# Optimization experiments

Measured on AMD Instinct MI355X. Metric: run time of the kernel, lower is better.

## Reference

```python
import jax, jax.numpy as jnp
import numpy as np

EMD_DIM = 64
NB_EMD = 512


def setup_inputs() -> dict:
    key = jax.random.key(0)
    k_x, k_e = jax.random.split(key)
    x = jax.random.normal(k_x, (32, 64, 64, EMD_DIM), dtype=jnp.float32)
    # codebook buffer, shape [emd_dim, nb_emd] as in the torch module
    embed = jax.random.normal(k_e, (EMD_DIM, NB_EMD), dtype=jnp.float32)
    return {"x": x, "embed": embed}


def reference(x, embed):
    # Eval-mode forward (the EMA buffer update only runs under self.training
    # and does not affect this forward's outputs).
    flatten = x.reshape(-1, EMD_DIM)                      # [N, d]
    dist = (jnp.sum(flatten * flatten, axis=1, keepdims=True)
            - 2.0 * flatten @ embed
            + jnp.sum(embed * embed, axis=0, keepdims=True))  # [N, K]
    emd_id_flat = jnp.argmax(-dist, axis=1)               # nearest code index [N]
    emd_id = emd_id_flat.reshape(x.shape[:-1])            # [B, H, W]
    q = jnp.take(embed.T, emd_id, axis=0)                 # gather codes -> [B,H,W,d]
    diff = jnp.mean((jax.lax.stop_gradient(q) - x) ** 2)  # commitment loss
    q_st = x + jax.lax.stop_gradient(q - x)               # straight-through
    return (q_st, diff, emd_id)
```

## Files before the change

### kernel.cpp

```cpp
#include <hip/hip_runtime.h>

#define N_VEC 131072
#define K 512
#define D 64
#define GUARD 0.05f
#define NB_GATHER 2048
#define FB_Q 16

typedef __attribute__((ext_vector_type(8))) short bf16x8;
typedef __attribute__((ext_vector_type(4))) float f32x4;

#define PIN(v) asm("" : "+v"(v))

static __device__ __forceinline__ short f2bf(float f) {
  unsigned u = __builtin_bit_cast(unsigned, f);
  u += 0x7fffu + ((u >> 16) & 1u);
  return (short)(u >> 16);
}
static __device__ __forceinline__ float bf2f(short h) {
  unsigned u = ((unsigned)(unsigned short)h) << 16;
  return __builtin_bit_cast(float, u);
}
static __device__ __forceinline__ void split8(const float4 f0, const float4 f1,
                                              bf16x8& h, bf16x8& m) {
  const float v[8] = {f0.x, f0.y, f0.z, f0.w, f1.x, f1.y, f1.z, f1.w};
#pragma unroll
  for (int j = 0; j < 8; ++j) {
    const short hh = f2bf(v[j]);
    h[j] = hh;
    m[j] = f2bf(v[j] - bf2f(hh));
  }
}

__global__ __launch_bounds__(64) void vq_prep_kernel(
    const float* __restrict__ embed, float* __restrict__ et,
    float* __restrict__ nrm, bf16x8* __restrict__ F, int* __restrict__ cnt)
{
  const int b = blockIdx.x;
  const int lane = threadIdx.x;
  if (b < 32) {
    const int row = lane & 15;
    const int kg  = lane >> 4;
    const int code = b * 16 + row;
#pragma unroll
    for (int c = 0; c < 2; ++c) {
      bf16x8 h, m;
#pragma unroll
      for (int j = 0; j < 8; ++j) {
        const int d = kg * 8 + c * 32 + j;
        const float e = embed[d * K + code];
        const short hh = f2bf(e);
        h[j] = hh;
        m[j] = f2bf(e - bf2f(hh));
      }
      F[b * 256 + c * 128 + 0  + lane] = h;
      F[b * 256 + c * 128 + 64 + lane] = m;
    }
  } else {
    if (b == 32 && lane == 0) cnt[0] = 0;
    const int code = (b - 32) * 64 + lane;
    float s = 0.f;
#pragma unroll
    for (int d = 0; d < D; ++d) {
      const float e = embed[d * K + code];
      et[code * D + d] = e;
      s = fmaf(e, e, s);
    }
    nrm[code] = s;
  }
}

#define MFMA12(P0, Q0, P1, Q1, BH0, BM0, BH1, BM1) do {                        \
    P0 = __builtin_amdgcn_mfma_f32_16x16x32_bf16(Ah0c0, BH0, kZero, 0, 0, 0); \
    P1 = __builtin_amdgcn_mfma_f32_16x16x32_bf16(Ah1c0, BH0, kZero, 0, 0, 0); \
    Q0 = __builtin_amdgcn_mfma_f32_16x16x32_bf16(Ah0c1, BM1, kZero, 0, 0, 0); \
    Q1 = __builtin_amdgcn_mfma_f32_16x16x32_bf16(Ah1c1, BM1, kZero, 0, 0, 0); \
    P0 = __builtin_amdgcn_mfma_f32_16x16x32_bf16(Ah0c1, BH1, P0, 0, 0, 0);    \
    P1 = __builtin_amdgcn_mfma_f32_16x16x32_bf16(Ah1c1, BH1, P1, 0, 0, 0);    \
    Q0 = __builtin_amdgcn_mfma_f32_16x16x32_bf16(Am0c0, BH0, Q0, 0, 0, 0);    \
    Q1 = __builtin_amdgcn_mfma_f32_16x16x32_bf16(Am1c0, BH0, Q1, 0, 0, 0);    \
    P0 = __builtin_amdgcn_mfma_f32_16x16x32_bf16(Ah0c0, BM0, P0, 0, 0, 0);    \
    P1 = __builtin_amdgcn_mfma_f32_16x16x32_bf16(Ah1c0, BM0, P1, 0, 0, 0);    \
    Q0 = __builtin_amdgcn_mfma_f32_16x16x32_bf16(Am0c1, BH1, Q0, 0, 0, 0);    \
    Q1 = __builtin_amdgcn_mfma_f32_16x16x32_bf16(Am1c1, BH1, Q1, 0, 0, 0);    \
  } while (0)

#define SCORE4(P0, Q0, P1, Q1, CODE, NV) do {                                  \
    _Pragma("unroll")                                                          \
    for (int r = 0; r < 4; ++r) {                                              \
      const float s0 = fmaf(-2.f, P0[r], fmaf(-2.f, Q0[r], (NV)));             \
      b2[r] = __builtin_amdgcn_fmed3f(s0, b1[r], b2[r]);                       \
      if (s0 < b1[r]) { b1[r] = s0; i1[r] = (CODE); }                          \
      const float s1 = fmaf(-2.f, P1[r], fmaf(-2.f, Q1[r], (NV)));             \
      b2[4 + r] = __builtin_amdgcn_fmed3f(s1, b1[4 + r], b2[4 + r]);           \
      if (s1 < b1[4 + r]) { b1[4 + r] = s1; i1[4 + r] = (CODE); }              \
    }                                                                          \
  } while (0)

__global__ __launch_bounds__(64, 4) void vq_coarse_kernel(
    const float* __restrict__ x, const bf16x8* __restrict__ F,
    const float* __restrict__ nrm, float* __restrict__ idf,
    int* __restrict__ cnt, int* __restrict__ list)
{
  const int lane = threadIdx.x;
  const int wid  = blockIdx.x;
  const int qbase = wid * 32;
  const int row = lane & 15;
  const int kg  = lane >> 4;

  bf16x8 Ah0c0, Ah0c1, Ah1c0, Ah1c1, Am0c0, Am0c1, Am1c0, Am1c1;
  {
    const float* xr0 = x + (size_t)(qbase + row) * D + kg * 8;
    const float* xr1 = x + (size_t)(qbase + 16 + row) * D + kg * 8;
    split8(*reinterpret_cast<const float4*>(xr0),
           *reinterpret_cast<const float4*>(xr0 + 4), Ah0c0, Am0c0);
    split8(*reinterpret_cast<const float4*>(xr0 + 32),
           *reinterpret_cast<const float4*>(xr0 + 36), Ah0c1, Am0c1);
    split8(*reinterpret_cast<const float4*>(xr1),
           *reinterpret_cast<const float4*>(xr1 + 4), Ah1c0, Am1c0);
    split8(*reinterpret_cast<const float4*>(xr1 + 32),
           *reinterpret_cast<const float4*>(xr1 + 36), Ah1c1, Am1c1);
  }

  float b1[8], b2[8]; int i1[8];
#pragma unroll
  for (int r = 0; r < 8; ++r) { b1[r] = 3.4e38f; b2[r] = 3.4e38f; i1[r] = 0; }

  f32x4 kZero = {0.f, 0.f, 0.f, 0.f};
  PIN(kZero);

  const bf16x8* fp = F + lane;
  bf16x8 Bh0 = fp[0], Bm0 = fp[64], Bh1 = fp[128], Bm1 = fp[192];
  fp += 256;
  const float* np = nrm + row;
  float nv = np[0];
  np += 16;

#pragma unroll 1
  for (int t = 0; t < 32; ++t) {
    bf16x8 nh0, nm0, nh1, nm1; float nvn;
    if (t < 31) {
      nh0 = fp[0]; nm0 = fp[64]; nh1 = fp[128]; nm1 = fp[192]; fp += 256;
      nvn = np[0]; np += 16;
    }

    f32x4 p0, q0, p1, q1;
    MFMA12(p0, q0, p1, q1, Bh0, Bm0, Bh1, Bm1);
    PIN(p0); PIN(q0); PIN(p1); PIN(q1);

    SCORE4(p0, q0, p1, q1, t * 16 + row, nv);
    Bh0 = nh0; Bm0 = nm0; Bh1 = nh1; Bm1 = nm1; nv = nvn;
  }

#pragma unroll
  for (int m = 1; m < 16; m <<= 1) {
#pragma unroll
    for (int r = 0; r < 8; ++r) {
      const float o1 = __shfl_xor(b1[r], m, 64);
      const int   oi = __shfl_xor(i1[r], m, 64);
      const float o2 = __shfl_xor(b2[r], m, 64);
      if (o1 < b1[r]) { b2[r] = fminf(b1[r], o2); b1[r] = o1; i1[r] = oi; }
      else            { b2[r] = fminf(b2[r], o1); }
    }
  }

  unsigned m32 = 0;
  if (row == 0) {
#pragma unroll
    for (int r = 0; r < 8; ++r) {
      const int qoff = (r >> 2) * 16 + kg * 4 + (r & 3);
      idf[qbase + qoff] = (float)i1[r];
      if (b2[r] - b1[r] < GUARD) m32 |= 1u << qoff;
    }
  }
  m32 |= __shfl_xor((int)m32, 16, 64);
  m32 |= __shfl_xor((int)m32, 32, 64);
  if (lane == 0 && m32) {
    int base = atomicAdd(cnt, __popc(m32));
    while (m32) {
      const int b = __ffs(m32) - 1;
      m32 &= m32 - 1;
      list[base++] = qbase + b;
    }
  }
}

__global__ __launch_bounds__(256) void vq_fallback_kernel(
    const float* __restrict__ x, const float* __restrict__ embed,
    const float* __restrict__ nrm, const int* __restrict__ cnt,
    const int* __restrict__ list, float* __restrict__ idf)
{
  __shared__ float x_lds[FB_Q * D];
  __shared__ int   s_qidx[FB_Q];
  __shared__ float s_best[4][FB_Q];
  __shared__ int   s_bid[4][FB_Q];
  const int tid  = threadIdx.x;
  const int lane = tid & 63;
  const int wv   = tid >> 6;
  const int n = cnt[0];

  for (int qb = blockIdx.x * FB_Q; qb < n; qb += gridDim.x * FB_Q) {
    __syncthreads();
    if (tid < FB_Q) {
      const int idx = qb + tid;
      s_qidx[tid] = list[idx < n ? idx : qb];
    }
    __syncthreads();
    {
      const int qj = tid >> 4, dq = tid & 15;
      *reinterpret_cast<float4*>(&x_lds[qj * D + dq * 4]) =
          *reinterpret_cast<const float4*>(x + (size_t)s_qidx[qj] * D + dq * 4);
    }
    __syncthreads();

    const int c0 = wv * 128 + lane;
    const int c1 = c0 + 64;
    float a0[FB_Q], a1[FB_Q];
#pragma unroll
    for (int i = 0; i < FB_Q; ++i) { a0[i] = 0.f; a1[i] = 0.f; }

#pragma unroll 4
    for (int ch = 0; ch < 16; ++ch) {
      const int d0 = ch * 4;
      const float e00 = embed[(d0 + 0) * K + c0];
      const float e01 = embed[(d0 + 0) * K + c1];
      const float e10 = embed[(d0 + 1) * K + c0];
      const float e11 = embed[(d0 + 1) * K + c1];
      const float e20 = embed[(d0 + 2) * K + c0];
      const float e21 = embed[(d0 + 2) * K + c1];
      const float e30 = embed[(d0 + 3) * K + c0];
      const float e31 = embed[(d0 + 3) * K + c1];
#pragma unroll
      for (int i = 0; i < FB_Q; ++i) {
        const float4 xv = *reinterpret_cast<const float4*>(&x_lds[i * D + d0]);
        a0[i] = fmaf(xv.x, e00, a0[i]);
        a0[i] = fmaf(xv.y, e10, a0[i]);
        a0[i] = fmaf(xv.z, e20, a0[i]);
        a0[i] = fmaf(xv.w, e30, a0[i]);
        a1[i] = fmaf(xv.x, e01, a1[i]);
        a1[i] = fmaf(xv.y, e11, a1[i]);
        a1[i] = fmaf(xv.z, e21, a1[i]);
        a1[i] = fmaf(xv.w, e31, a1[i]);
      }
    }

    const float nr0 = nrm[c0], nr1 = nrm[c1];
#pragma unroll
    for (int i = 0; i < FB_Q; ++i) {
      float best; int bid;
      const float s0 = fmaf(-2.f, a0[i], nr0);
      best = s0; bid = c0;
      const float s1 = fmaf(-2.f, a1[i], nr1);
      if (s1 < best) { best = s1; bid = c1; }
#pragma unroll
      for (int off = 32; off > 0; off >>= 1) {
        const float s2 = __shfl_down(best, off, 64);
        const int   b2 = __shfl_down(bid, off, 64);
        if (s2 < best || (s2 == best && b2 < bid)) { best = s2; bid = b2; }
      }
      if (lane == 0) { s_best[wv][i] = best; s_bid[wv][i] = bid; }
    }
    __syncthreads();
    if (tid < FB_Q) {
      float best = s_best[0][tid]; int bid = s_bid[0][tid];
#pragma unroll
      for (int w = 1; w < 4; ++w) {
        const float s = s_best[w][tid];
        if (s < best) { best = s; bid = s_bid[w][tid]; }
      }
      idf[s_qidx[tid]] = (float)bid;
    }
  }
}

__global__ __launch_bounds__(256) void vq_gather_kernel(
    const float* __restrict__ x, const float* __restrict__ et,
    const float* __restrict__ idf, float* __restrict__ q,
    float* __restrict__ partial)
{
  const int tid = blockIdx.x * 256 + threadIdx.x;
  const int stride = gridDim.x * 256;
  float acc = 0.f;
  for (int idx = tid; idx < N_VEC * (D / 4); idx += stride) {
    const int v = idx >> 4;
    const int d4 = idx & 15;
    const int id = (int)idf[v];
    const float4 xv = reinterpret_cast<const float4*>(x)[idx];
    const float4 ev = reinterpret_cast<const float4*>(et)[(id << 4) + d4];
    const float e0 = ev.x - xv.x, e1 = ev.y - xv.y, e2 = ev.z - xv.z, e3 = ev.w - xv.w;
    acc += (e0 * e0 + e1 * e1) + (e2 * e2 + e3 * e3);
    reinterpret_cast<float4*>(q)[idx] = ev;
  }
  acc += __shfl_down(acc, 32, 64);
  acc += __shfl_down(acc, 16, 64);
  acc += __shfl_down(acc, 8, 64);
  acc += __shfl_down(acc, 4, 64);
  acc += __shfl_down(acc, 2, 64);
  acc += __shfl_down(acc, 1, 64);
  __shared__ float sred[4];
  if ((threadIdx.x & 63) == 0) sred[threadIdx.x >> 6] = acc;
  __syncthreads();
  if (threadIdx.x == 0)
    partial[blockIdx.x] = (sred[0] + sred[1]) + (sred[2] + sred[3]);
}

__global__ __launch_bounds__(256) void vq_finalize_kernel(
    const float* __restrict__ partial, float* __restrict__ out)
{
  float acc = 0.f;
  for (int i = threadIdx.x; i < NB_GATHER; i += 256) acc += partial[i];
  acc += __shfl_down(acc, 32, 64);
  acc += __shfl_down(acc, 16, 64);
  acc += __shfl_down(acc, 8, 64);
  acc += __shfl_down(acc, 4, 64);
  acc += __shfl_down(acc, 2, 64);
  acc += __shfl_down(acc, 1, 64);
  __shared__ float sred[4];
  if ((threadIdx.x & 63) == 0) sred[threadIdx.x >> 6] = acc;
  __syncthreads();
  if (threadIdx.x == 0)
    out[0] = ((sred[0] + sred[1]) + (sred[2] + sred[3])) * (1.0f / (float)(N_VEC * D));
}

extern "C" void kernel_launch(void* const* d_in, const int* in_sizes, int n_in,
                              void* d_out, int out_size, void* d_ws, size_t ws_size,
                              hipStream_t stream) {
  const float* x = (const float*)d_in[0];
  const float* embed = (const float*)d_in[1];
  float* out = (float*)d_out;
  float* q    = out;
  float* diff = out + 8388608;
  float* idf  = out + 8388609;

  float* ws = (float*)d_ws;
  float* et      = ws;
  float* nrm     = ws + 32768;
  float* partial = ws + 33312;
  int*   cnt     = (int*)(ws + 35360);
  int*   list    = (int*)(ws + 35368);
  bf16x8* F = (bf16x8*)(ws + 35368 + N_VEC);

  vq_prep_kernel<<<40, 64, 0, stream>>>(embed, et, nrm, F, cnt);
  vq_coarse_kernel<<<N_VEC / 32, 64, 0, stream>>>(x, F, nrm, idf, cnt, list);
  vq_fallback_kernel<<<1024, 256, 0, stream>>>(x, embed, nrm, cnt, list, idf);
  vq_gather_kernel<<<NB_GATHER, 256, 0, stream>>>(x, et, idf, q, partial);
  vq_finalize_kernel<<<1, 256, 0, stream>>>(partial, diff);
}
```

Measured before the change: 85.09 us.

## Stage codebook fragments in LDS shared by 8 waves per block

The coarse VQ kernel now runs 8 waves per 512-thread block. Each block cooperatively copies half of the bf16 hi/mid codebook fragment array (64 KB) into shared memory in two phases, and every wave reads its MFMA B operands from LDS instead of each wave streaming them from global/L2. This cuts redundant global codebook traffic per wave. In exchange it adds block-wide barriers, drops the explicit register prefetch and asm pinning, and the 64 KB LDS use may limit occupancy.

```diff
diff --git a/kernel.cpp b/kernel.cpp
--- a/kernel.cpp
+++ b/kernel.cpp
@@ -9,8 +9,6 @@
 
 typedef __attribute__((ext_vector_type(8))) short bf16x8;
 typedef __attribute__((ext_vector_type(4))) float f32x4;
-
-#define PIN(v) asm("" : "+v"(v))
 
 static __device__ __forceinline__ short f2bf(float f) {
   unsigned u = __builtin_bit_cast(unsigned, f);
@@ -97,16 +95,18 @@
     }                                                                          \
   } while (0)
 
-__global__ __launch_bounds__(64, 4) void vq_coarse_kernel(
+__global__ __launch_bounds__(512, 4) void vq_coarse_kernel(
     const float* __restrict__ x, const bf16x8* __restrict__ F,
     const float* __restrict__ nrm, float* __restrict__ idf,
     int* __restrict__ cnt, int* __restrict__ list)
 {
-  const int lane = threadIdx.x;
-  const int wid  = blockIdx.x;
-  const int qbase = wid * 32;
-  const int row = lane & 15;
-  const int kg  = lane >> 4;
+  __shared__ bf16x8 LB[4096];
+  const int tid  = threadIdx.x;
+  const int lane = tid & 63;
+  const int w    = tid >> 6;
+  const int row  = lane & 15;
+  const int kg   = lane >> 4;
+  const int qbase = blockIdx.x * 256 + w * 32;
 
   bf16x8 Ah0c0, Ah0c1, Ah1c0, Ah1c1, Am0c0, Am0c1, Am1c0, Am1c1;
   {
@@ -126,30 +126,31 @@
 #pragma unroll
   for (int r = 0; r < 8; ++r) { b1[r] = 3.4e38f; b2[r] = 3.4e38f; i1[r] = 0; }
 
-  f32x4 kZero = {0.f, 0.f, 0.f, 0.f};
-  PIN(kZero);
-
-  const bf16x8* fp = F + lane;
-  bf16x8 Bh0 = fp[0], Bm0 = fp[64], Bh1 = fp[128], Bm1 = fp[192];
-  fp += 256;
-  const float* np = nrm + row;
-  float nv = np[0];
-  np += 16;
+  const f32x4 kZero = {0.f, 0.f, 0.f, 0.f};
 
 #pragma unroll 1
-  for (int t = 0; t < 32; ++t) {
-    bf16x8 nh0, nm0, nh1, nm1; float nvn;
-    if (t < 31) {
-      nh0 = fp[0]; nm0 = fp[64]; nh1 = fp[128]; nm1 = fp[192]; fp += 256;
-      nvn = np[0]; np += 16;
-    }
-
-    f32x4 p0, q0, p1, q1;
-    MFMA12(p0, q0, p1, q1, Bh0, Bm0, Bh1, Bm1);
-    PIN(p0); PIN(q0); PIN(p1); PIN(q1);
-
-    SCORE4(p0, q0, p1, q1, t * 16 + row, nv);
-    Bh0 = nh0; Bm0 = nm0; Bh1 = nh1; Bm1 = nm1; nv = nvn;
+  for (int ph = 0; ph < 2; ++ph) {
+    if (ph) __syncthreads();
+    {
+      const float4* src = reinterpret_cast<const float4*>(F + ph * 4096);
+      float4* dst = reinterpret_cast<float4*>(LB);
+#pragma unroll
+      for (int j = 0; j < 8; ++j) dst[tid + j * 512] = src[tid + j * 512];
+    }
+    __syncthreads();
+
+#pragma unroll 4
+    for (int t = 0; t < 16; ++t) {
+      const bf16x8 Bh0 = LB[t * 256 + lane];
+      const bf16x8 Bm0 = LB[t * 256 + 64 + lane];
+      const bf16x8 Bh1 = LB[t * 256 + 128 + lane];
+      const bf16x8 Bm1 = LB[t * 256 + 192 + lane];
+      const int code = (ph * 16 + t) * 16 + row;
+      const float nv = nrm[code];
+      f32x4 p0, q0, p1, q1;
+      MFMA12(p0, q0, p1, q1, Bh0, Bm0, Bh1, Bm1);
+      SCORE4(p0, q0, p1, q1, code, nv);
+    }
   }
 
 #pragma unroll
@@ -341,7 +342,7 @@
   bf16x8* F = (bf16x8*)(ws + 35368 + N_VEC);
 
   vq_prep_kernel<<<40, 64, 0, stream>>>(embed, et, nrm, F, cnt);
-  vq_coarse_kernel<<<N_VEC / 32, 64, 0, stream>>>(x, F, nrm, idf, cnt, list);
+  vq_coarse_kernel<<<N_VEC / 256, 512, 0, stream>>>(x, F, nrm, idf, cnt, list);
   vq_fallback_kernel<<<1024, 256, 0, stream>>>(x, embed, nrm, cnt, list, idf);
   vq_gather_kernel<<<NB_GATHER, 256, 0, stream>>>(x, et, idf, q, partial);
   vq_finalize_kernel<<<1, 256, 0, stream>>>(partial, diff);
```

Result: faster. 80.77 us (-5.1%).
